# Performance work log

Measured on AMD Instinct MI355X. Metric: run time of the kernel, lower is better.

The kernel has to match this reference:

```python
import math
import jax, jax.numpy as jnp
import numpy as np

EMB_DIM, EMB_KS, EMB_HS = 64, 2, 1
H, CS = 4, 32  # n_heads, GLA chunk size
EPS = 1e-5


def _ln4d(x, g, b):
    # LayerNormalization4D: normalize over channel dim (axis 1), biased var
    mu = x.mean(1, keepdims=True)
    var = ((x - mu) ** 2).mean(1, keepdims=True)
    return (x - mu) / jnp.sqrt(var + EPS) * g + b


def _unfold(x):
    # x [N,C,Q] -> [N, L, C*ks]; torch F.unfold feature order is c-major, k-minor
    N, C, Q = x.shape
    L = (Q - EMB_KS) // EMB_HS + 1
    f = jnp.stack([x[:, :, k:k + L] for k in range(EMB_KS)], axis=2)  # [N,C,ks,L]
    return f.reshape(N, C * EMB_KS, L).transpose(0, 2, 1)


def _deconv1d(x, w, b):
    # ConvTranspose1d, stride=EMB_HS=1; x [N,Cin,L], w [Cin,Cout,K]
    N, Cin, L = x.shape
    Cout, K = w.shape[1], w.shape[2]
    out_len = (L - 1) * EMB_HS + K
    y = jnp.zeros((N, Cout, out_len), x.dtype)
    for k in range(K):
        y = y.at[:, :, k:k + L].add(jnp.einsum('ncl,co->nol', x, w[:, :, k]))
    return y + b[None, :, None]


def _gla(x, Wq, Wk, Wv, Wg1, Wg2, Wr, gn, Wo):
    # chunked gated linear attention (use_gk=True, use_gv=False, swish output gate)
    N, L, D = x.shape
    Dk = Wq.shape[1] // H
    Dv = Wv.shape[1] // H
    Lp = -(-L // CS) * CS
    pad = Lp - L
    nc = Lp // CS
    q = (x @ Wq) * (Dk ** -0.5)
    k = x @ Wk
    v = x @ Wv
    gk = jax.nn.log_sigmoid((x @ Wg1) @ Wg2) / 32.0  # gate_logit_normalizer=32

    def chunk(t, dh):
        t = jnp.pad(t, ((0, 0), (0, pad), (0, 0)))
        return t.reshape(N, nc, CS, H, dh)

    q, k, gk, v = chunk(q, Dk), chunk(k, Dk), chunk(gk, Dk), chunk(v, Dv)
    gc = jnp.cumsum(gk, axis=2)                      # within-chunk log-decay [N,nc,CS,H,Dk]
    q_i = q * jnp.exp(gc)
    k_i = k * jnp.exp(-gc)
    mask = jnp.tril(jnp.ones((CS, CS), bool))
    A = jnp.einsum('ncthd,ncshd->nchts', q_i, k_i)   # intra-chunk scores
    A = jnp.where(mask[None, None, None], A, 0.0)
    o_intra = jnp.einsum('nchts,ncshd->ncthd', A, v)
    gl = gc[:, :, -1]                                 # chunk-total log decay [N,nc,H,Dk]
    k_o = k * jnp.exp(gl[:, :, None] - gc)

    def step(S, inp):
        qi, ko, vc, g = inp
        o = jnp.einsum('nthk,nhkv->nthv', qi, S)      # inter-chunk contribution
        S = S * jnp.exp(g)[..., None] + jnp.einsum('nthk,nthv->nhkv', ko, vc)
        return S, o

    S0 = jnp.zeros((N, H, Dk, Dv), x.dtype)
    xs = tuple(jnp.moveaxis(t, 1, 0) for t in (q_i, k_o, v, gl))
    _, o_inter = jax.lax.scan(step, S0, xs)
    o = (o_intra + jnp.moveaxis(o_inter, 0, 1)).reshape(N, Lp, H, Dv)[:, :L]
    # per-head RMSNorm + swish output gate
    o = o / jnp.sqrt(jnp.mean(o * o, -1, keepdims=True) + EPS) * gn.reshape(H, Dv)
    r = x @ Wr
    o = o.reshape(N, L, H * Dv) * (r * jax.nn.sigmoid(r))
    return o @ Wo


def _forward(x, mouth, intra_gamma, intra_beta, intra_Wq, intra_Wk, intra_Wv,
             intra_Wg1, intra_Wg2, intra_Wr, intra_gn, intra_Wo, intra_ct_w, intra_ct_b,
             inter_gamma, inter_beta, inter_Wq, inter_Wk, inter_Wv,
             inter_Wg1, inter_Wg2, inter_Wr, inter_gn, inter_Wo, inter_ct_w, inter_ct_b):
    B, C, old_T, old_Q = x.shape
    T = math.ceil((old_T - EMB_KS) / EMB_HS) * EMB_HS + EMB_KS
    Q = math.ceil((old_Q - EMB_KS) / EMB_HS) * EMB_HS + EMB_KS
    x = jnp.pad(x, ((0, 0), (0, 0), (0, T - old_T), (0, Q - old_Q)))
    # intra (frequency) path
    u = _ln4d(x, intra_gamma, intra_beta)
    u = u.transpose(0, 2, 1, 3).reshape(B * T, C, Q)
    f = _unfold(u)                                    # [B*T, Q-1, C*ks]
    g = _gla(f, intra_Wq, intra_Wk, intra_Wv, intra_Wg1, intra_Wg2, intra_Wr, intra_gn, intra_Wo)
    y = _deconv1d(g.transpose(0, 2, 1), intra_ct_w, intra_ct_b)  # [B*T, C, Q]
    y = y.reshape(B, T, C, Q).transpose(0, 2, 1, 3) + x
    # inter (time) path
    u = _ln4d(y, inter_gamma, inter_beta)
    u = u.transpose(0, 3, 1, 2).reshape(B * Q, C, T)
    f = _unfold(u)                                    # [B*Q, T-1, C*ks]
    g = _gla(f, inter_Wq, inter_Wk, inter_Wv, inter_Wg1, inter_Wg2, inter_Wr, inter_gn, inter_Wo)
    z = _deconv1d(g.transpose(0, 2, 1), inter_ct_w, inter_ct_b)  # [B*Q, C, T]
    z = z.reshape(B, Q, C, T).transpose(0, 2, 3, 1) + y
    return z[..., :old_T, :old_Q]


def setup_inputs() -> dict:
    key = jax.random.key(0)
    ks = jax.random.split(key, 32)
    D = EMB_DIM * EMB_KS       # 128 = GLA d_model
    DKV = 2 * D                # 256 (expand_k = expand_v = 2)

    def w(i, shape, fan):
        return jax.random.normal(ks[i], shape, jnp.float32) / np.sqrt(fan).astype(np.float32)

    inp = {
        'x': jax.random.normal(ks[0], (4, EMB_DIM, 256, 128), jnp.float32),
        'mouth': jax.random.normal(ks[1], (4, 1, 64, 64), jnp.float32),
    }
    for p, base in (('intra', 2), ('inter', 14)):
        inp[p + '_gamma'] = jnp.ones((1, EMB_DIM, 1, 1), jnp.float32)
        inp[p + '_beta'] = jnp.zeros((1, EMB_DIM, 1, 1), jnp.float32)
        inp[p + '_Wq'] = w(base, (D, DKV), D)
        inp[p + '_Wk'] = w(base + 1, (D, DKV), D)
        inp[p + '_Wv'] = w(base + 2, (D, DKV), D)
        inp[p + '_Wg1'] = w(base + 3, (D, 32), D)
        inp[p + '_Wg2'] = w(base + 4, (32, DKV), 32)
        inp[p + '_Wr'] = w(base + 5, (D, DKV), D)
        inp[p + '_gn'] = jnp.ones((DKV,), jnp.float32)
        inp[p + '_Wo'] = w(base + 6, (DKV, D), DKV)
        inp[p + '_ct_w'] = w(base + 7, (D, EMB_DIM, EMB_KS), D * EMB_KS)
        inp[p + '_ct_b'] = jnp.zeros((EMB_DIM,), jnp.float32)
    return inp


def reference(x, mouth, intra_gamma, intra_beta, intra_Wq, intra_Wk, intra_Wv,
              intra_Wg1, intra_Wg2, intra_Wr, intra_gn, intra_Wo, intra_ct_w, intra_ct_b,
              inter_gamma, inter_beta, inter_Wq, inter_Wk, inter_Wv,
              inter_Wg1, inter_Wg2, inter_Wr, inter_gn, inter_Wo, inter_ct_w, inter_ct_b):
    return _forward(x, mouth, intra_gamma, intra_beta, intra_Wq, intra_Wk, intra_Wv,
                    intra_Wg1, intra_Wg2, intra_Wr, intra_gn, intra_Wo, intra_ct_w, intra_ct_b,
                    inter_gamma, inter_beta, inter_Wq, inter_Wk, inter_Wv,
                    inter_Wg1, inter_Wg2, inter_Wr, inter_gn, inter_Wo, inter_ct_w, inter_ct_b)
```

## Files before the change

### kernel.cpp

```cpp
#include <hip/hip_runtime.h>

#define EPS 1e-5f

__device__ __forceinline__ float logsig(float z) {
    return fminf(z, 0.0f) - log1pf(__expf(-fabsf(z)));
}

__global__ __launch_bounds__(256)
void pack_weights(const float* __restrict__ Wq0, const float* __restrict__ Wk0,
                  const float* __restrict__ Wv0, const float* __restrict__ Wr0,
                  const float* __restrict__ Wg10,
                  const float* __restrict__ Wq1, const float* __restrict__ Wk1,
                  const float* __restrict__ Wv1, const float* __restrict__ Wr1,
                  const float* __restrict__ Wg11,
                  float* __restrict__ pk)
{
    int idx = blockIdx.x * 256 + threadIdx.x;
    int p   = (idx >= 34816) ? 1 : 0;
    int j   = idx - p * 34816;
    const float* Wq  = p ? Wq1  : Wq0;
    const float* Wk  = p ? Wk1  : Wk0;
    const float* Wv  = p ? Wv1  : Wv0;
    const float* Wr  = p ? Wr1  : Wr0;
    const float* Wg1 = p ? Wg11 : Wg10;
    float* base = pk + p * 135168;
    if (j < 16384) {
        int cc = j >> 8, d = j & 255;
        float4 v = { Wq[(2*cc)*256 + d], Wq[(2*cc+1)*256 + d],
                     Wk[(2*cc)*256 + d], Wk[(2*cc+1)*256 + d] };
        ((float4*)base)[j] = v;
    } else if (j < 32768) {
        int jj = j - 16384;
        int cc = jj >> 8, d = jj & 255;
        float4 v = { Wv[(2*cc)*256 + d], Wv[(2*cc+1)*256 + d],
                     Wr[(2*cc)*256 + d], Wr[(2*cc+1)*256 + d] };
        ((float4*)(base + 65536))[jj] = v;
    } else {
        int jj = j - 32768;
        int cc = jj >> 5, m = jj & 31;
        float2 v = { Wg1[(2*cc)*32 + m], Wg1[(2*cc+1)*32 + m] };
        ((float2*)(base + 131072))[jj] = v;
    }
}

template<int SLEN, int PSTRIDE>
__global__ __launch_bounds__(512)
__attribute__((amdgpu_waves_per_eu(2, 2)))
void gla_pass(const float* __restrict__ src, float* __restrict__ out,
              const float* __restrict__ gamma, const float* __restrict__ beta,
              const float4* __restrict__ pWqk, const float4* __restrict__ pWvr,
              const float2* __restrict__ pWg1,
              const float* __restrict__ Wg2,
              const float* __restrict__ gn, const float* __restrict__ Wo,
              const float* __restrict__ ctw, const float* __restrict__ ctb)
{
    constexpr int NC = SLEN / 32;
    constexpr int L  = SLEN - 1;

    __shared__ __align__(16) float sxA[64][36];
    __shared__ __align__(16) float sxB[64][36];
    __shared__ __align__(16) float sxr[64][32];
    __shared__ __align__(16) float qf[32][256];
    __shared__ __align__(16) float kf[32][256];
    __shared__ __align__(16) float voc[32][256];
    __shared__ __align__(16) float uni[4608];
    __shared__ __align__(16) float fw1t[32][36];
    __shared__ __align__(16) float gprevs[128];
    __shared__ float egl[256];
    __shared__ float sgam[64], sbet[64];
    __shared__ float smu[33], sinv[33];
    __shared__ float gcarry[256];

    float* const Ats  = uni;
    float* const gdec = uni;

    const int tid  = threadIdx.x;
    const int lane = tid & 63;
    const int wv   = tid >> 6;
    const int h    = wv & 3;
    const int kh   = wv >> 2;
    const int d    = tid & 255;
    const int th   = (tid >> 8) & 1;
    const int n    = blockIdx.x;

    int b, fixedoff;
    if constexpr (PSTRIDE == 1) { b = n >> 8; fixedoff = (n & 255) * 128; }
    else                        { b = n >> 7; fixedoff = (n & 127); }
    const int cbase = (b * 64) * 32768 + fixedoff;

    if (tid < 64)  { sgam[tid] = gamma[tid]; sbet[tid] = beta[tid]; }
    if (tid < 128) gprevs[tid] = 0.0f;

    float S[32];
    #pragma unroll
    for (int k = 0; k < 32; ++k) S[k] = 0.0f;

    const float gnv  = gn[h * 64 + lane];
    const float bias = ctb[lane];

    #pragma unroll
    for (int k = 0; k < 5; ++k) {
        int idx = tid + k * 512;
        if (idx < 64 * 33) {
            int cc = idx / 33, i = idx - cc * 33;
            sxA[cc][i] = src[cbase + cc * 32768 + i * PSTRIDE];
        }
    }

    for (int ch = 0; ch < NC; ++ch) {
        const int l0 = ch * 32;
        float (* const cur)[36] = (ch & 1) ? sxB : sxA;
        float (* const nxt)[36] = (ch & 1) ? sxA : sxB;
        __syncthreads();

        float pre[5];
        const bool pf = (ch + 1 < NC);
        if (pf) {
            const int l0n = l0 + 32;
            #pragma unroll
            for (int k = 0; k < 5; ++k) {
                int idx = tid + k * 512;
                if (idx < 64 * 33) {
                    int cc = idx / 33, i = idx - cc * 33;
                    int p  = l0n + i; if (p > SLEN - 1) p = SLEN - 1;
                    pre[k] = src[cbase + cc * 32768 + p * PSTRIDE];
                }
            }
        }

        for (int cp = wv; cp < 17; cp += 8) {
            const int col = 2 * cp + (lane >> 5);
            float s1 = 0.0f, s2 = 0.0f;
            if (col < 33) {
                const int c0 = (lane & 31) * 2;
                float x0 = cur[c0][col], x1 = cur[c0 + 1][col];
                s1 = x0 + x1; s2 = x0 * x0 + x1 * x1;
            }
            #pragma unroll
            for (int off = 16; off > 0; off >>= 1) {
                s1 += __shfl_xor(s1, off, 64);
                s2 += __shfl_xor(s2, off, 64);
            }
            if ((lane & 31) == 0 && col < 33) {
                float mu  = s1 * (1.0f / 64.0f);
                float var = s2 * (1.0f / 64.0f) - mu * mu;
                smu[col]  = mu;
                sinv[col] = rsqrtf(fmaxf(var, 0.0f) + EPS);
            }
        }
        __syncthreads();

        #pragma unroll
        for (int k = 0; k < 5; ++k) {
            int idx = tid + k * 512;
            if (idx < 64 * 33) {
                int cc = idx / 33, i = idx - cc * 33;
                float x = cur[cc][i];
                if (i < 32) sxr[cc][i] = x;
                cur[cc][i] = (x - smu[i]) * sinv[i] * sgam[cc] + sbet[cc];
            }
        }
        __syncthreads();

        {
            const int m = tid & 31, tg2 = tid >> 5;
            float a0 = 0.0f, a1 = 0.0f;
            float2 wg = pWg1[m];
            #pragma unroll 2
            for (int cc = 0; cc < 64; ++cc) {
                float2 wn = pWg1[((cc + 1) & 63) * 32 + m];
                a0 += cur[cc][tg2]      * wg.x + cur[cc][tg2 + 1]  * wg.y;
                a1 += cur[cc][tg2 + 16] * wg.x + cur[cc][tg2 + 17] * wg.y;
                wg = wn;
            }
            fw1t[m][tg2] = a0; fw1t[m][tg2 + 16] = a1;
        }
        __syncthreads();

        float rn[16];
        {
            const int t0 = th * 16;
            float acc2[16];
            #pragma unroll
            for (int t = 0; t < 16; ++t) acc2[t] = 0.0f;
            for (int mm = 0; mm < 32; ++mm) {
                const float w = Wg2[mm * 256 + d];
                #pragma unroll
                for (int i = 0; i < 4; ++i) {
                    float4 f4 = *(const float4*)&fw1t[mm][t0 + 4 * i];
                    acc2[4*i+0] += f4.x * w; acc2[4*i+1] += f4.y * w;
                    acc2[4*i+2] += f4.z * w; acc2[4*i+3] += f4.w * w;
                }
            }
            float r = 0.0f;
            #pragma unroll
            for (int t = 0; t < 16; ++t) {
                if ((l0 + t0 + t) < L) r += logsig(acc2[t]) * (1.0f / 32.0f);
                acc2[t] = r;
            }
            if (th == 0) gcarry[d] = r;
            __syncthreads();
            const float c = (th == 0) ? 0.0f : gcarry[d];
            #pragma unroll
            for (int t = 0; t < 16; ++t) rn[t] = c + acc2[t];
            if (th == 1) egl[d] = __expf(rn[15]);
        }

        if (pf) {
            #pragma unroll
            for (int k = 0; k < 5; ++k) {
                int idx = tid + k * 512;
                if (idx < 64 * 33) {
                    int cc = idx / 33, i = idx - cc * 33;
                    nxt[cc][i] = pre[k];
                }
            }
        }

        {
            const int t0 = th * 16;
            float aq[16], ak[16];
            #pragma unroll
            for (int t = 0; t < 16; ++t) { aq[t] = 0.0f; ak[t] = 0.0f; }
            float4 w = pWqk[d];
            for (int cc = 0; cc < 64; ++cc) {
                float4 wn = pWqk[((cc + 1) & 63) * 256 + d];
                float col[17];
                #pragma unroll
                for (int i = 0; i < 4; ++i) {
                    float4 c4 = *(const float4*)&cur[cc][t0 + 4 * i];
                    col[4*i] = c4.x; col[4*i+1] = c4.y; col[4*i+2] = c4.z; col[4*i+3] = c4.w;
                }
                col[16] = cur[cc][t0 + 16];
                #pragma unroll
                for (int t = 0; t < 16; ++t) {
                    aq[t] += col[t] * w.x + col[t+1] * w.y;
                    ak[t] += col[t] * w.z + col[t+1] * w.w;
                }
                w = wn;
            }
            #pragma unroll
            for (int t = 0; t < 16; ++t) {
                bool valid = (l0 + t0 + t) < L;
                qf[t0 + t][d] = valid ? aq[t] * 0.125f * __expf(rn[t]) : 0.0f;
                kf[t0 + t][d] = valid ? ak[t] * __expf(-rn[t]) : 0.0f;
            }
        }
        {
            const int t0 = th * 16;
            float av[16];
            #pragma unroll
            for (int t = 0; t < 16; ++t) av[t] = 0.0f;
            float4 w = pWvr[d];
            for (int cc = 0; cc < 64; ++cc) {
                float4 wn = pWvr[((cc + 1) & 63) * 256 + d];
                float col[17];
                #pragma unroll
                for (int i = 0; i < 4; ++i) {
                    float4 c4 = *(const float4*)&cur[cc][t0 + 4 * i];
                    col[4*i] = c4.x; col[4*i+1] = c4.y; col[4*i+2] = c4.z; col[4*i+3] = c4.w;
                }
                col[16] = cur[cc][t0 + 16];
                #pragma unroll
                for (int t = 0; t < 16; ++t) av[t] += col[t] * w.x + col[t+1] * w.y;
                w = wn;
            }
            #pragma unroll
            for (int t = 0; t < 16; ++t)
                voc[t0 + t][d] = ((l0 + t0 + t) < L) ? av[t] : 0.0f;
        }
        __syncthreads();

        const int base = h * 64;
        float vcol[32];
        #pragma unroll
        for (int t = 0; t < 32; ++t) vcol[t] = voc[t][base + lane];

        for (int pi = lane + 64 * kh; pi < 528; pi += 128) {
            float fpi = (float)pi;
            int t = (int)((sqrtf(8.0f * fpi + 1.0f) - 1.0f) * 0.5f);
            if (((t + 1) * (t + 2)) / 2 <= pi) ++t;
            if ((t * (t + 1)) / 2 > pi) --t;
            int s = pi - (t * (t + 1)) / 2;
            float a = 0.0f;
            #pragma unroll
            for (int ii = 0; ii < 16; ++ii) {
                int i = (ii + lane) & 15;
                float4 q4 = *(const float4*)&qf[t][base + 4 * i];
                float4 k4 = *(const float4*)&kf[s][base + 4 * i];
                a += q4.x*k4.x + q4.y*k4.y + q4.z*k4.z + q4.w*k4.w;
            }
            Ats[h * 1152 + t * 36 + s] = a;
        }
        __syncthreads();

        if (kh == 1) {
            #pragma unroll
            for (int t = 0; t < 32; ++t) {
                float oe = 0.0f;
                #pragma unroll
                for (int i = 0; i < 8; ++i) {
                    float4 q4 = *(const float4*)&qf[t][base + 32 + 4 * i];
                    oe += q4.x*S[4*i] + q4.y*S[4*i+1] + q4.z*S[4*i+2] + q4.w*S[4*i+3];
                }
                voc[t][base + lane] = oe;
            }
        }
        __syncthreads();

        if (kh == 0) {
            #pragma unroll
            for (int t = 0; t < 32; ++t) {
                float ot = voc[t][base + lane];
                #pragma unroll
                for (int i = 0; i < 8; ++i) {
                    float4 q4 = *(const float4*)&qf[t][base + 4 * i];
                    ot += q4.x*S[4*i] + q4.y*S[4*i+1] + q4.z*S[4*i+2] + q4.w*S[4*i+3];
                }
                const float* arow = &Ats[h * 1152 + t * 36];
                #pragma unroll
                for (int s4 = 0; s4 + 4 <= t + 1; s4 += 4) {
                    float4 a4 = *(const float4*)&arow[s4];
                    ot += a4.x*vcol[s4] + a4.y*vcol[s4+1] + a4.z*vcol[s4+2] + a4.w*vcol[s4+3];
                }
                #pragma unroll
                for (int s = (t + 1) & ~3; s <= t; ++s) ot += arow[s] * vcol[s];
                float ss = ot * ot;
                #pragma unroll
                for (int off = 32; off > 0; off >>= 1) ss += __shfl_xor(ss, off, 64);
                voc[t][base + lane] = ot * rsqrtf(ss * (1.0f / 64.0f) + EPS) * gnv;
            }
        } else {
            const int kb = base + 32;
            #pragma unroll
            for (int i = 0; i < 8; ++i) {
                float s0 = 0.0f, s1 = 0.0f, s2 = 0.0f, s3 = 0.0f;
                #pragma unroll
                for (int t = 0; t < 32; ++t) {
                    float4 k4 = *(const float4*)&kf[t][kb + 4 * i];
                    const float vt = vcol[t];
                    s0 += k4.x * vt; s1 += k4.y * vt; s2 += k4.z * vt; s3 += k4.w * vt;
                }
                S[4*i+0] = egl[kb + 4*i+0] * (S[4*i+0] + s0);
                S[4*i+1] = egl[kb + 4*i+1] * (S[4*i+1] + s1);
                S[4*i+2] = egl[kb + 4*i+2] * (S[4*i+2] + s2);
                S[4*i+3] = egl[kb + 4*i+3] * (S[4*i+3] + s3);
            }
        }
        __syncthreads();

        if (kh == 0) {
            const int kb = base;
            #pragma unroll
            for (int i = 0; i < 8; ++i) {
                float s0 = 0.0f, s1 = 0.0f, s2 = 0.0f, s3 = 0.0f;
                #pragma unroll
                for (int t = 0; t < 32; ++t) {
                    float4 k4 = *(const float4*)&kf[t][kb + 4 * i];
                    const float vt = vcol[t];
                    s0 += k4.x * vt; s1 += k4.y * vt; s2 += k4.z * vt; s3 += k4.w * vt;
                }
                S[4*i+0] = egl[kb + 4*i+0] * (S[4*i+0] + s0);
                S[4*i+1] = egl[kb + 4*i+1] * (S[4*i+1] + s1);
                S[4*i+2] = egl[kb + 4*i+2] * (S[4*i+2] + s2);
                S[4*i+3] = egl[kb + 4*i+3] * (S[4*i+3] + s3);
            }
        }

        {
            const int t0 = th * 16;
            float ar[16];
            #pragma unroll
            for (int t = 0; t < 16; ++t) ar[t] = 0.0f;
            float4 w = pWvr[d];
            for (int cc = 0; cc < 64; ++cc) {
                float4 wn = pWvr[((cc + 1) & 63) * 256 + d];
                float col[17];
                #pragma unroll
                for (int i = 0; i < 4; ++i) {
                    float4 c4 = *(const float4*)&cur[cc][t0 + 4 * i];
                    col[4*i] = c4.x; col[4*i+1] = c4.y; col[4*i+2] = c4.z; col[4*i+3] = c4.w;
                }
                col[16] = cur[cc][t0 + 16];
                #pragma unroll
                for (int t = 0; t < 16; ++t) ar[t] += col[t] * w.z + col[t+1] * w.w;
                w = wn;
            }
            #pragma unroll
            for (int t = 0; t < 16; ++t) {
                const float r = ar[t];
                voc[t0 + t][d] *= r / (1.0f + __expf(-r));
            }
        }
        __syncthreads();

        {
            const int m2  = tid & 63;
            const int tg4 = tid >> 6;
            float accA[4] = {0,0,0,0}, accB[4] = {0,0,0,0};
            for (int j = 0; j < 256; j += 4) {
                float wA0 = Wo[(j+0)*128 + m2],      wB0 = Wo[(j+0)*128 + m2 + 64];
                float wA1 = Wo[(j+1)*128 + m2],      wB1 = Wo[(j+1)*128 + m2 + 64];
                float wA2 = Wo[(j+2)*128 + m2],      wB2 = Wo[(j+2)*128 + m2 + 64];
                float wA3 = Wo[(j+3)*128 + m2],      wB3 = Wo[(j+3)*128 + m2 + 64];
                #pragma unroll
                for (int i = 0; i < 4; ++i) {
                    float4 o4 = *(const float4*)&voc[tg4 * 4 + i][j];
                    accA[i] += o4.x*wA0 + o4.y*wA1 + o4.z*wA2 + o4.w*wA3;
                    accB[i] += o4.x*wB0 + o4.y*wB1 + o4.z*wB2 + o4.w*wB3;
                }
            }
            #pragma unroll
            for (int i = 0; i < 4; ++i) {
                gdec[(tg4 * 4 + i) * 132 + m2]      = accA[i];
                gdec[(tg4 * 4 + i) * 132 + m2 + 64] = accB[i];
            }
        }
        __syncthreads();

        {
            const int o  = lane;
            const int pg = wv;
            const float2* ctw2 = (const float2*)ctw;
            float acc4[4] = {0,0,0,0};
            for (int c4 = 0; c4 < 128; c4 += 4) {
                float2 w0 = ctw2[(c4+0)*64 + o];
                float2 w1 = ctw2[(c4+1)*64 + o];
                float2 w2 = ctw2[(c4+2)*64 + o];
                float2 w3 = ctw2[(c4+3)*64 + o];
                float4 r[5];
                r[0] = (pg == 0) ? *(const float4*)&gprevs[c4]
                                 : *(const float4*)&gdec[(pg*4 - 1) * 132 + c4];
                #pragma unroll
                for (int j = 0; j < 4; ++j)
                    r[j+1] = *(const float4*)&gdec[(pg*4 + j) * 132 + c4];
                #pragma unroll
                for (int i = 0; i < 4; ++i) {
                    acc4[i] += r[i+1].x*w0.x + r[i].x*w0.y
                             + r[i+1].y*w1.x + r[i].y*w1.y
                             + r[i+1].z*w2.x + r[i].z*w2.y
                             + r[i+1].w*w3.x + r[i].w*w3.y;
                }
            }
            #pragma unroll
            for (int i = 0; i < 4; ++i) {
                const int tl = pg * 4 + i;
                const int oi = cbase + o * 32768 + (l0 + tl) * PSTRIDE;
                out[oi] = acc4[i] + bias + sxr[o][tl];
            }
        }
        __syncthreads();
        if (tid < 128) gprevs[tid] = gdec[31 * 132 + tid];
    }
}

extern "C" void kernel_launch(void* const* d_in, const int* in_sizes, int n_in,
                              void* d_out, int out_size, void* d_ws, size_t ws_size,
                              hipStream_t stream)
{
    const float* x = (const float*)d_in[0];
    float* y  = (float*)d_ws;
    float* pk = (float*)d_ws + 8388608;
    float* z  = (float*)d_out;

    pack_weights<<<dim3(272), dim3(256), 0, stream>>>(
        (const float*)d_in[4],  (const float*)d_in[5],  (const float*)d_in[6],
        (const float*)d_in[9],  (const float*)d_in[7],
        (const float*)d_in[16], (const float*)d_in[17], (const float*)d_in[18],
        (const float*)d_in[21], (const float*)d_in[19],
        pk);

    gla_pass<128, 1><<<dim3(1024), dim3(512), 0, stream>>>(
        x, y,
        (const float*)d_in[2],  (const float*)d_in[3],
        (const float4*)pk, (const float4*)(pk + 65536), (const float2*)(pk + 131072),
        (const float*)d_in[8],
        (const float*)d_in[10], (const float*)d_in[11],
        (const float*)d_in[12], (const float*)d_in[13]);

    gla_pass<256, 128><<<dim3(512), dim3(512), 0, stream>>>(
        y, z,
        (const float*)d_in[14], (const float*)d_in[15],
        (const float4*)(pk + 135168), (const float4*)(pk + 135168 + 65536),
        (const float2*)(pk + 135168 + 131072),
        (const float*)d_in[20],
        (const float*)d_in[22], (const float*)d_in[23],
        (const float*)d_in[24], (const float*)d_in[25]);
}
```

Before: 5.953 ms.

## Fuse q/k/v projections, pre-transpose Wo, and drop waves-per-eu constraint

```diff
diff --git a/kernel.cpp b/kernel.cpp
--- a/kernel.cpp
+++ b/kernel.cpp
@@ -9,21 +9,22 @@
 __global__ __launch_bounds__(256)
 void pack_weights(const float* __restrict__ Wq0, const float* __restrict__ Wk0,
                   const float* __restrict__ Wv0, const float* __restrict__ Wr0,
-                  const float* __restrict__ Wg10,
+                  const float* __restrict__ Wg10, const float* __restrict__ Wo0,
                   const float* __restrict__ Wq1, const float* __restrict__ Wk1,
                   const float* __restrict__ Wv1, const float* __restrict__ Wr1,
-                  const float* __restrict__ Wg11,
+                  const float* __restrict__ Wg11, const float* __restrict__ Wo1,
                   float* __restrict__ pk)
 {
     int idx = blockIdx.x * 256 + threadIdx.x;
-    int p   = (idx >= 34816) ? 1 : 0;
-    int j   = idx - p * 34816;
+    int p   = (idx >= 43008) ? 1 : 0;
+    int j   = idx - p * 43008;
     const float* Wq  = p ? Wq1  : Wq0;
     const float* Wk  = p ? Wk1  : Wk0;
     const float* Wv  = p ? Wv1  : Wv0;
     const float* Wr  = p ? Wr1  : Wr0;
     const float* Wg1 = p ? Wg11 : Wg10;
-    float* base = pk + p * 135168;
+    const float* Wo  = p ? Wo1  : Wo0;
+    float* base = pk + p * 167936;
     if (j < 16384) {
         int cc = j >> 8, d = j & 255;
         float4 v = { Wq[(2*cc)*256 + d], Wq[(2*cc+1)*256 + d],
@@ -35,23 +36,28 @@
         float4 v = { Wv[(2*cc)*256 + d], Wv[(2*cc+1)*256 + d],
                      Wr[(2*cc)*256 + d], Wr[(2*cc+1)*256 + d] };
         ((float4*)(base + 65536))[jj] = v;
-    } else {
+    } else if (j < 34816) {
         int jj = j - 32768;
         int cc = jj >> 5, m = jj & 31;
         float2 v = { Wg1[(2*cc)*32 + m], Wg1[(2*cc+1)*32 + m] };
         ((float2*)(base + 131072))[jj] = v;
+    } else {
+        int jj = j - 34816;
+        int m2 = jj >> 6, jb = jj & 63;
+        float4 v = { Wo[(4*jb+0)*128 + m2], Wo[(4*jb+1)*128 + m2],
+                     Wo[(4*jb+2)*128 + m2], Wo[(4*jb+3)*128 + m2] };
+        ((float4*)(base + 135168))[jj] = v;
     }
 }
 
 template<int SLEN, int PSTRIDE>
 __global__ __launch_bounds__(512)
-__attribute__((amdgpu_waves_per_eu(2, 2)))
 void gla_pass(const float* __restrict__ src, float* __restrict__ out,
               const float* __restrict__ gamma, const float* __restrict__ beta,
               const float4* __restrict__ pWqk, const float4* __restrict__ pWvr,
-              const float2* __restrict__ pWg1,
+              const float2* __restrict__ pWg1, const float4* __restrict__ WoT4,
               const float* __restrict__ Wg2,
-              const float* __restrict__ gn, const float* __restrict__ Wo,
+              const float* __restrict__ gn,
               const float* __restrict__ ctw, const float* __restrict__ ctb)
 {
     constexpr int NC = SLEN / 32;
@@ -62,7 +68,7 @@
     __shared__ __align__(16) float sxr[64][32];
     __shared__ __align__(16) float qf[32][256];
     __shared__ __align__(16) float kf[32][256];
-    __shared__ __align__(16) float voc[32][256];
+    __shared__ __align__(16) float voc[32][260];
     __shared__ __align__(16) float uni[4608];
     __shared__ __align__(16) float fw1t[32][36];
     __shared__ __align__(16) float gprevs[128];
@@ -128,20 +134,15 @@
             }
         }
 
-        for (int cp = wv; cp < 17; cp += 8) {
-            const int col = 2 * cp + (lane >> 5);
-            float s1 = 0.0f, s2 = 0.0f;
-            if (col < 33) {
-                const int c0 = (lane & 31) * 2;
-                float x0 = cur[c0][col], x1 = cur[c0 + 1][col];
-                s1 = x0 + x1; s2 = x0 * x0 + x1 * x1;
-            }
-            #pragma unroll
-            for (int off = 16; off > 0; off >>= 1) {
+        for (int col = wv; col < 33; col += 8) {
+            float x = cur[lane][col];
+            float s1 = x, s2 = x * x;
+            #pragma unroll
+            for (int off = 32; off > 0; off >>= 1) {
                 s1 += __shfl_xor(s1, off, 64);
                 s2 += __shfl_xor(s2, off, 64);
             }
-            if ((lane & 31) == 0 && col < 33) {
+            if (lane == 0) {
                 float mu  = s1 * (1.0f / 64.0f);
                 float var = s2 * (1.0f / 64.0f) - mu * mu;
                 smu[col]  = mu;
@@ -165,13 +166,11 @@
         {
             const int m = tid & 31, tg2 = tid >> 5;
             float a0 = 0.0f, a1 = 0.0f;
-            float2 wg = pWg1[m];
             #pragma unroll 2
             for (int cc = 0; cc < 64; ++cc) {
-                float2 wn = pWg1[((cc + 1) & 63) * 32 + m];
+                float2 wg = pWg1[cc * 32 + m];
                 a0 += cur[cc][tg2]      * wg.x + cur[cc][tg2 + 1]  * wg.y;
                 a1 += cur[cc][tg2 + 16] * wg.x + cur[cc][tg2 + 17] * wg.y;
-                wg = wn;
             }
             fw1t[m][tg2] = a0; fw1t[m][tg2 + 16] = a1;
         }
@@ -217,57 +216,37 @@
             }
         }
 
-        {
-            const int t0 = th * 16;
-            float aq[16], ak[16];
-            #pragma unroll
-            for (int t = 0; t < 16; ++t) { aq[t] = 0.0f; ak[t] = 0.0f; }
-            float4 w = pWqk[d];
+        #pragma unroll
+        for (int p = 0; p < 2; ++p) {
+            const int t0 = th * 16 + p * 8;
+            float aq[8], ak[8], av[8];
+            #pragma unroll
+            for (int t = 0; t < 8; ++t) { aq[t] = 0.0f; ak[t] = 0.0f; av[t] = 0.0f; }
             for (int cc = 0; cc < 64; ++cc) {
-                float4 wn = pWqk[((cc + 1) & 63) * 256 + d];
-                float col[17];
-                #pragma unroll
-                for (int i = 0; i < 4; ++i) {
-                    float4 c4 = *(const float4*)&cur[cc][t0 + 4 * i];
-                    col[4*i] = c4.x; col[4*i+1] = c4.y; col[4*i+2] = c4.z; col[4*i+3] = c4.w;
-                }
-                col[16] = cur[cc][t0 + 16];
-                #pragma unroll
-                for (int t = 0; t < 16; ++t) {
-                    aq[t] += col[t] * w.x + col[t+1] * w.y;
-                    ak[t] += col[t] * w.z + col[t+1] * w.w;
-                }
-                w = wn;
-            }
-            #pragma unroll
-            for (int t = 0; t < 16; ++t) {
-                bool valid = (l0 + t0 + t) < L;
-                qf[t0 + t][d] = valid ? aq[t] * 0.125f * __expf(rn[t]) : 0.0f;
-                kf[t0 + t][d] = valid ? ak[t] * __expf(-rn[t]) : 0.0f;
-            }
-        }
-        {
-            const int t0 = th * 16;
-            float av[16];
-            #pragma unroll
-            for (int t = 0; t < 16; ++t) av[t] = 0.0f;
-            float4 w = pWvr[d];
-            for (int cc = 0; cc < 64; ++cc) {
-                float4 wn = pWvr[((cc + 1) & 63) * 256 + d];
-                float col[17];
-                #pragma unroll
-                for (int i = 0; i < 4; ++i) {
-                    float4 c4 = *(const float4*)&cur[cc][t0 + 4 * i];
-                    col[4*i] = c4.x; col[4*i+1] = c4.y; col[4*i+2] = c4.z; col[4*i+3] = c4.w;
-                }
-                col[16] = cur[cc][t0 + 16];
-                #pragma unroll
-                for (int t = 0; t < 16; ++t) av[t] += col[t] * w.x + col[t+1] * w.y;
-                w = wn;
-            }
-            #pragma unroll
-            for (int t = 0; t < 16; ++t)
-                voc[t0 + t][d] = ((l0 + t0 + t) < L) ? av[t] : 0.0f;
+                float col[9];
+                float4 c4 = *(const float4*)&cur[cc][t0];
+                float4 c5 = *(const float4*)&cur[cc][t0 + 4];
+                col[0]=c4.x; col[1]=c4.y; col[2]=c4.z; col[3]=c4.w;
+                col[4]=c5.x; col[5]=c5.y; col[6]=c5.z; col[7]=c5.w;
+                col[8]=cur[cc][t0 + 8];
+                float4 wqk = pWqk[cc * 256 + d];
+                float4 wvr = pWvr[cc * 256 + d];
+                #pragma unroll
+                for (int t = 0; t < 8; ++t) {
+                    aq[t] += col[t] * wqk.x + col[t+1] * wqk.y;
+                    ak[t] += col[t] * wqk.z + col[t+1] * wqk.w;
+                    av[t] += col[t] * wvr.x + col[t+1] * wvr.y;
+                }
+            }
+            #pragma unroll
+            for (int t = 0; t < 8; ++t) {
+                const int tt = t0 + t;
+                bool valid = (l0 + tt) < L;
+                float r = rn[p * 8 + t];
+                qf[tt][d]  = valid ? aq[t] * 0.125f * __expf(r) : 0.0f;
+                kf[tt][d]  = valid ? ak[t] * __expf(-r) : 0.0f;
+                voc[tt][d] = valid ? av[t] : 0.0f;
+            }
         }
         __syncthreads();
 
@@ -372,9 +351,8 @@
             float ar[16];
             #pragma unroll
             for (int t = 0; t < 16; ++t) ar[t] = 0.0f;
-            float4 w = pWvr[d];
             for (int cc = 0; cc < 64; ++cc) {
-                float4 wn = pWvr[((cc + 1) & 63) * 256 + d];
+                float4 w = pWvr[cc * 256 + d];
                 float col[17];
                 #pragma unroll
                 for (int i = 0; i < 4; ++i) {
@@ -384,7 +362,6 @@
                 col[16] = cur[cc][t0 + 16];
                 #pragma unroll
                 for (int t = 0; t < 16; ++t) ar[t] += col[t] * w.z + col[t+1] * w.w;
-                w = wn;
             }
             #pragma unroll
             for (int t = 0; t < 16; ++t) {
@@ -395,25 +372,29 @@
         __syncthreads();
 
         {
-            const int m2  = tid & 63;
-            const int tg4 = tid >> 6;
+            const int cg = tid & 31;
+            const int rg = tid >> 5;
             float accA[4] = {0,0,0,0}, accB[4] = {0,0,0,0};
-            for (int j = 0; j < 256; j += 4) {
-                float wA0 = Wo[(j+0)*128 + m2],      wB0 = Wo[(j+0)*128 + m2 + 64];
-                float wA1 = Wo[(j+1)*128 + m2],      wB1 = Wo[(j+1)*128 + m2 + 64];
-                float wA2 = Wo[(j+2)*128 + m2],      wB2 = Wo[(j+2)*128 + m2 + 64];
-                float wA3 = Wo[(j+3)*128 + m2],      wB3 = Wo[(j+3)*128 + m2 + 64];
-                #pragma unroll
-                for (int i = 0; i < 4; ++i) {
-                    float4 o4 = *(const float4*)&voc[tg4 * 4 + i][j];
-                    accA[i] += o4.x*wA0 + o4.y*wA1 + o4.z*wA2 + o4.w*wA3;
-                    accB[i] += o4.x*wB0 + o4.y*wB1 + o4.z*wB2 + o4.w*wB3;
-                }
-            }
-            #pragma unroll
-            for (int i = 0; i < 4; ++i) {
-                gdec[(tg4 * 4 + i) * 132 + m2]      = accA[i];
-                gdec[(tg4 * 4 + i) * 132 + m2 + 64] = accB[i];
+            for (int jb = 0; jb < 64; ++jb) {
+                float4 w0 = WoT4[(cg*4+0)*64 + jb];
+                float4 w1 = WoT4[(cg*4+1)*64 + jb];
+                float4 w2 = WoT4[(cg*4+2)*64 + jb];
+                float4 w3 = WoT4[(cg*4+3)*64 + jb];
+                float4 oa = *(const float4*)&voc[rg*2    ][4*jb];
+                float4 ob = *(const float4*)&voc[rg*2 + 1][4*jb];
+                accA[0] += oa.x*w0.x + oa.y*w0.y + oa.z*w0.z + oa.w*w0.w;
+                accA[1] += oa.x*w1.x + oa.y*w1.y + oa.z*w1.z + oa.w*w1.w;
+                accA[2] += oa.x*w2.x + oa.y*w2.y + oa.z*w2.z + oa.w*w2.w;
+                accA[3] += oa.x*w3.x + oa.y*w3.y + oa.z*w3.z + oa.w*w3.w;
+                accB[0] += ob.x*w0.x + ob.y*w0.y + ob.z*w0.z + ob.w*w0.w;
+                accB[1] += ob.x*w1.x + ob.y*w1.y + ob.z*w1.z + ob.w*w1.w;
+                accB[2] += ob.x*w2.x + ob.y*w2.y + ob.z*w2.z + ob.w*w2.w;
+                accB[3] += ob.x*w3.x + ob.y*w3.y + ob.z*w3.z + ob.w*w3.w;
+            }
+            #pragma unroll
+            for (int c = 0; c < 4; ++c) {
+                gdec[(rg*2    ) * 132 + cg*4 + c] = accA[c];
+                gdec[(rg*2 + 1) * 132 + cg*4 + c] = accB[c];
             }
         }
         __syncthreads();
@@ -463,27 +444,29 @@
     float* pk = (float*)d_ws + 8388608;
     float* z  = (float*)d_out;
 
-    pack_weights<<<dim3(272), dim3(256), 0, stream>>>(
+    pack_weights<<<dim3(336), dim3(256), 0, stream>>>(
         (const float*)d_in[4],  (const float*)d_in[5],  (const float*)d_in[6],
-        (const float*)d_in[9],  (const float*)d_in[7],
+        (const float*)d_in[9],  (const float*)d_in[7],  (const float*)d_in[11],
         (const float*)d_in[16], (const float*)d_in[17], (const float*)d_in[18],
-        (const float*)d_in[21], (const float*)d_in[19],
+        (const float*)d_in[21], (const float*)d_in[19], (const float*)d_in[23],
         pk);
 
     gla_pass<128, 1><<<dim3(1024), dim3(512), 0, stream>>>(
         x, y,
         (const float*)d_in[2],  (const float*)d_in[3],
         (const float4*)pk, (const float4*)(pk + 65536), (const float2*)(pk + 131072),
+        (const float4*)(pk + 135168),
         (const float*)d_in[8],
-        (const float*)d_in[10], (const float*)d_in[11],
+        (const float*)d_in[10],
         (const float*)d_in[12], (const float*)d_in[13]);
 
     gla_pass<256, 128><<<dim3(512), dim3(512), 0, stream>>>(
         y, z,
         (const float*)d_in[14], (const float*)d_in[15],
-        (const float4*)(pk + 135168), (const float4*)(pk + 135168 + 65536),
-        (const float2*)(pk + 135168 + 131072),
+        (const float4*)(pk + 167936), (const float4*)(pk + 167936 + 65536),
+        (const float2*)(pk + 167936 + 131072),
+        (const float4*)(pk + 167936 + 135168),
         (const float*)d_in[20],
-        (const float*)d_in[22], (const float*)d_in[23],
+        (const float*)d_in[22],
         (const float*)d_in[24], (const float*)d_in[25]);
 }
```

New measurement: 7.462 ms. +25.4%, slower.
